# Optimization experiments

Hardware: AMD Instinct MI355X
Metric: run time of the kernel (lower is better)

The kernel has to match this reference:

```python
import jax, jax.numpy as jnp
import numpy as np

SIGMA = 0.05
KSIZE = 3
MIN_VAL = 50.0
MAX_VAL = 100.0


def _gauss_kernel():
    # ax = range(-(3//2)+1, 3//2+1) = [-1, 0, 1]  (matches TF int-floor-div)
    ax = jnp.arange(-(KSIZE // 2) + 1.0, KSIZE // 2 + 1.0)
    xx, yy = jnp.meshgrid(ax, ax)
    k = jnp.exp(-(xx ** 2 + yy ** 2) / (2.0 * SIGMA ** 2))
    k = k / jnp.sum(k)
    return k[..., None, None].astype(jnp.float32)  # HWIO, C=1


def _reflect_pad(x):
    return jnp.pad(x, ((0, 0), (1, 1), (1, 1), (0, 0)), mode='reflect')


def _conv(x, k):
    return jax.lax.conv_general_dilated(x, k, (1, 1), 'VALID',
                                        dimension_numbers=('NHWC', 'HWIO', 'NHWC'))


def _canny(images):
    blur = _conv(_reflect_pad(images), _gauss_kernel())
    h = jnp.array([[-1, 0, 1], [-2, 0, 2], [-1, 0, 1]], jnp.float32)[..., None, None]
    v = jnp.array([[-1, -2, -1], [0, 0, 0], [1, 2, 1]], jnp.float32)[..., None, None]
    bp = _reflect_pad(blur)
    gx = _conv(bp, h)
    gy = _conv(bp, v)
    gxy = jnp.sqrt(gx ** 2 + gy ** 2)
    # NOTE: original uses atan2(gx, gy) in this arg order
    theta = (jnp.arctan2(gx, gy) * (180.0 / np.pi) + 90.0) % 180.0

    H, W = gx.shape[1], gx.shape[2]
    # dilation2d with a -inf/0 kernel == max over the kernel's zero-offsets of the
    # zero-padded image; offsets are (dy,dx) of the 0 entries of each 3x3 filter.
    offsets = [
        [(1, 0), (1, 1), (1, 2)],  # horizontal bin: middle row
        [(0, 2), (1, 1), (2, 0)],  # 45 deg: anti-diagonal
        [(0, 1), (1, 1), (2, 1)],  # vertical bin: middle column
        [(0, 0), (1, 1), (2, 2)],  # 135 deg: main diagonal
    ]
    conds = [
        jnp.logical_or(theta >= 157.5, theta < 22.5),
        jnp.logical_and(theta >= 22.5, theta < 67.5),
        jnp.logical_and(theta >= 67.5, theta < 112.5),
        jnp.logical_and(theta >= 112.5, theta < 157.5),
    ]

    edge = jnp.zeros_like(gxy)
    for cond, offs in zip(conds, offsets):
        ang = jnp.where(cond, gxy, 0.0)
        pad = jnp.pad(ang, ((0, 0), (1, 1), (1, 1), (0, 0)))  # zero pad, as ZeroPadding2D
        mp = pad[:, offs[0][0]:offs[0][0] + H, offs[0][1]:offs[0][1] + W, :]
        for dy, dx in offs[1:]:
            mp = jnp.maximum(mp, pad[:, dy:dy + H, dx:dx + W, :])
        edge = edge + jnp.where(mp == ang, ang, 0.0)

    edge_sure = jnp.where(edge >= MAX_VAL, 255.0, 0.0)
    edge_week = jnp.where(jnp.logical_and(edge >= MIN_VAL, edge < MAX_VAL), 255.0, 0.0)
    edge_image = jnp.where(jnp.logical_or(edge_week == 255.0, edge_sure == 255.0), 255.5, 0.0)
    return edge_image, edge_week, edge_sure


def setup_inputs() -> dict:
    key = jax.random.key(0)
    images = jax.random.uniform(key, (16, 1024, 1024, 1), dtype=jnp.float32) * 255.0
    return {"images": images}


def reference(images):
    return _canny(images)
```

## Files before the change

### kernel.cpp

```cpp
#include <hip/hip_runtime.h>
#include <math.h>

#define IMG_H 1024
#define IMG_W 1024
#define OUT_H 1025
#define OUT_W 1025
#define NIMG  16
#define TOTAL (NIMG * OUT_H * OUT_W)

#define TILE_W 64
#define TILE_H 16
#define HALO_W 68
#define HALO_H 18
#define NQX    17
#define NQUAD  (HALO_H * NQX)
#define NTHREADS 320

__device__ __forceinline__ int refl(int k) {
    if (k >= 2) return (k <= 1025) ? (k - 2) : 1022;
    return k;
}

__device__ __forceinline__ void sobel_generic(const float* __restrict__ img, int i, int j,
                                              float& gx, float& gy) {
    int r0 = refl(i), r1 = refl(i + 1), r2 = refl(i + 2);
    int c0 = refl(j), c1 = refl(j + 1), c2 = refl(j + 2);
    const float* p0 = img + r0 * IMG_W;
    const float* p1 = img + r1 * IMG_W;
    const float* p2 = img + r2 * IMG_W;
    float v00 = p0[c0], v01 = p0[c1], v02 = p0[c2];
    float v10 = p1[c0],               v12 = p1[c2];
    float v20 = p2[c0], v21 = p2[c1], v22 = p2[c2];

    float t = -v00;
    t = __fadd_rn(t, v02);
    t = __fadd_rn(t, -2.0f * v10);
    t = __fadd_rn(t, 2.0f * v12);
    t = __fadd_rn(t, -v20);
    gx = __fadd_rn(t, v22);

    t = -v00;
    t = __fadd_rn(t, -2.0f * v01);
    t = __fadd_rn(t, -v02);
    t = __fadd_rn(t, v20);
    t = __fadd_rn(t, 2.0f * v21);
    gy = __fadd_rn(t, v22);
}

__device__ int classify_slow(float gx, float gy) {
    float t = (float)atan2((double)gx, (double)gy);
    float deg = __fmul_rn(t, (float)(180.0 / M_PI));
    float th = __fadd_rn(deg, 90.0f);
    th = fmodf(th, 180.0f);
    if (th < 0.0f) th += 180.0f;
    if (th < 22.5f || th >= 157.5f) return 0;
    if (th < 67.5f) return 1;
    if (th < 112.5f) return 2;
    return 3;
}

__device__ __forceinline__ int classify(float gx, float gy) {
    float ax = fabsf(gx), ay = fabsf(gy);
    const float T22_LO = 0.414172141e0f;
    const float T22_HI = 0.414254984e0f;
    const float T67_LO = 2.413972141e0f;
    const float T67_HI = 2.414454984e0f;

    if (ax <= ay * T22_LO) return 2;
    if (ax >= ay * T67_HI) return 0;
    if (ax >= ay * T22_HI && ax <= ay * T67_LO) {
        unsigned s = (__float_as_uint(gx) ^ __float_as_uint(gy)) >> 31;
        return s ? 1 : 3;
    }
    return classify_slow(gx, gy);
}

__device__ __forceinline__ float mag(float gx, float gy) {
    return __fsqrt_rn(__fadd_rn(__fmul_rn(gx, gx), __fmul_rn(gy, gy)));
}

__device__ __forceinline__ void load6(const float* __restrict__ p, float v[6]) {
    float4 a = *(const float4*)p;
    float2 b = *(const float2*)(p + 4);
    v[0] = a.x; v[1] = a.y; v[2] = a.z; v[3] = a.w; v[4] = b.x; v[5] = b.y;
}

__global__ __launch_bounds__(NTHREADS) void canny_kernel(const float* __restrict__ images,
                                                         float* __restrict__ out) {
    __shared__ float    g_s[HALO_H * HALO_W];
    __shared__ unsigned b_u[HALO_H * NQX];

    const int tile_ox = blockIdx.x * TILE_W;
    const int tile_oy = blockIdx.y * TILE_H;
    const int n       = blockIdx.z;
    const float* img = images + (size_t)n * IMG_H * IMG_W;
    const int t = threadIdx.x;

    if (t < NQUAD) {
        int hy  = t / NQX;
        int qx  = t - hy * NQX;
        int oy  = tile_oy + hy - 1;
        int ox0 = tile_ox + qx * 4 - 2;

        float    gq[4];
        unsigned bq[4];

        if (oy >= 2 && oy <= 1023 && ox0 >= 2 && ox0 <= 1020) {
            const float* r0p = img + (oy - 2) * IMG_W + (ox0 - 2);
            float R0[6], R1[6], R2[6];
            load6(r0p, R0);
            load6(r0p + IMG_W, R1);
            load6(r0p + 2 * IMG_W, R2);
            #pragma unroll
            for (int p = 0; p < 4; p++) {
                float v00 = R0[p], v01 = R0[p + 1], v02 = R0[p + 2];
                float v10 = R1[p],                  v12 = R1[p + 2];
                float v20 = R2[p], v21 = R2[p + 1], v22 = R2[p + 2];

                float s = -v00;
                s = __fadd_rn(s, v02);
                s = __fadd_rn(s, -2.0f * v10);
                s = __fadd_rn(s, 2.0f * v12);
                s = __fadd_rn(s, -v20);
                float gx = __fadd_rn(s, v22);

                s = -v00;
                s = __fadd_rn(s, -2.0f * v01);
                s = __fadd_rn(s, -v02);
                s = __fadd_rn(s, v20);
                s = __fadd_rn(s, 2.0f * v21);
                float gy = __fadd_rn(s, v22);

                gq[p] = mag(gx, gy);
                bq[p] = (unsigned)classify(gx, gy);
            }
        } else {
            #pragma unroll
            for (int p = 0; p < 4; p++) {
                int ox = ox0 + p;
                float g = -1.0f;
                unsigned b = 255u;
                if (oy >= 0 && oy < OUT_H && ox >= 0 && ox < OUT_W) {
                    float gx, gy;
                    sobel_generic(img, oy, ox, gx, gy);
                    g = mag(gx, gy);
                    b = (unsigned)classify(gx, gy);
                }
                gq[p] = g;
                bq[p] = b;
            }
        }

        int ldoff = hy * HALO_W + qx * 4;
        *(float4*)&g_s[ldoff] = make_float4(gq[0], gq[1], gq[2], gq[3]);
        b_u[hy * NQX + qx] = bq[0] | (bq[1] << 8) | (bq[2] << 16) | (bq[3] << 24);
    }
    __syncthreads();

    const unsigned char* b_s = (const unsigned char*)b_u;
    #pragma unroll
    for (int q = 0; q < 4; q++) {
        int p = t + NTHREADS * q;
        if (p >= TILE_W * TILE_H) break;
        int r = p >> 6, c = p & 63;
        int oy = tile_oy + r, ox = tile_ox + c;
        if (oy >= OUT_H || ox >= OUT_W) continue;

        int hc = (r + 1) * HALO_W + (c + 2);
        float gc = g_s[hc];
        int   bc = b_s[hc];

        int doff = (bc == 0) ? 1
                 : (bc == 1) ? (HALO_W - 1)
                 : (bc == 2) ? HALO_W
                 :             (HALO_W + 1);

        float nmax = 0.0f;
        float g1 = g_s[hc + doff];
        if (b_s[hc + doff] == bc && g1 > nmax) nmax = g1;
        float g2 = g_s[hc - doff];
        if (b_s[hc - doff] == bc && g2 > nmax) nmax = g2;

        float e = (gc >= nmax) ? gc : 0.0f;

        size_t o = (size_t)(n * OUT_H + oy) * OUT_W + ox;
        out[o]                       = (e >= 50.0f) ? 255.5f : 0.0f;
        out[(size_t)TOTAL + o]       = (e >= 50.0f && e < 100.0f) ? 255.0f : 0.0f;
        out[(size_t)(2 * TOTAL) + o] = (e >= 100.0f) ? 255.0f : 0.0f;
    }
}

extern "C" void kernel_launch(void* const* d_in, const int* in_sizes, int n_in,
                              void* d_out, int out_size, void* d_ws, size_t ws_size,
                              hipStream_t stream) {
    const float* images = (const float*)d_in[0];
    float* out = (float*)d_out;
    dim3 grid((OUT_W + TILE_W - 1) / TILE_W,
              (OUT_H + TILE_H - 1) / TILE_H,
              NIMG);
    canny_kernel<<<grid, NTHREADS, 0, stream>>>(images, out);
}
```

Before: 297.8 us.

## Compute two Sobel rows per thread and vectorize NMS phase over 4 pixels

Each producer thread now loads four input rows and computes gradient magnitude and bin for two halo rows, reusing the shared middle rows. This cuts global loads per gradient and lowers the thread count to 256. The NMS phase has each thread handle four consecutive pixels: it reads float4 magnitudes and packed bin words from shared memory and picks neighbors with selects instead of per-pixel scattered byte loads. The classify function is restructured so the slow atan2 path is a single unlikely branch. The trade-off is more registers per thread and only 153 of 256 threads active in the gradient phase.

```diff
diff --git a/kernel.cpp b/kernel.cpp
--- a/kernel.cpp
+++ b/kernel.cpp
@@ -6,15 +6,15 @@
 #define OUT_H 1025
 #define OUT_W 1025
 #define NIMG  16
-#define TOTAL (NIMG * OUT_H * OUT_W)
+#define TOTAL ((size_t)NIMG * OUT_H * OUT_W)
 
 #define TILE_W 64
 #define TILE_H 16
 #define HALO_W 68
 #define HALO_H 18
 #define NQX    17
-#define NQUAD  (HALO_H * NQX)
-#define NTHREADS 320
+#define NPAIRS 9
+#define NMT    (NQX * NPAIRS)
 
 __device__ __forceinline__ int refl(int k) {
     if (k >= 2) return (k <= 1025) ? (k - 2) : 1022;
@@ -47,6 +47,28 @@
     gy = __fadd_rn(t, v22);
 }
 
+__device__ __forceinline__ void sobel_rows(const float R0[6], const float R1[6],
+                                           const float R2[6], int p,
+                                           float& gx, float& gy) {
+    float v00 = R0[p], v01 = R0[p + 1], v02 = R0[p + 2];
+    float v10 = R1[p],                  v12 = R1[p + 2];
+    float v20 = R2[p], v21 = R2[p + 1], v22 = R2[p + 2];
+
+    float s = -v00;
+    s = __fadd_rn(s, v02);
+    s = __fadd_rn(s, -2.0f * v10);
+    s = __fadd_rn(s, 2.0f * v12);
+    s = __fadd_rn(s, -v20);
+    gx = __fadd_rn(s, v22);
+
+    s = -v00;
+    s = __fadd_rn(s, -2.0f * v01);
+    s = __fadd_rn(s, -v02);
+    s = __fadd_rn(s, v20);
+    s = __fadd_rn(s, 2.0f * v21);
+    gy = __fadd_rn(s, v22);
+}
+
 __device__ int classify_slow(float gx, float gy) {
     float t = (float)atan2((double)gx, (double)gy);
     float deg = __fmul_rn(t, (float)(180.0 / M_PI));
@@ -66,13 +88,14 @@
     const float T67_LO = 2.413972141e0f;
     const float T67_HI = 2.414454984e0f;
 
-    if (ax <= ay * T22_LO) return 2;
-    if (ax >= ay * T67_HI) return 0;
-    if (ax >= ay * T22_HI && ax <= ay * T67_LO) {
-        unsigned s = (__float_as_uint(gx) ^ __float_as_uint(gy)) >> 31;
-        return s ? 1 : 3;
-    }
-    return classify_slow(gx, gy);
+    bool in22 = (ax > ay * T22_LO) && (ax < ay * T22_HI);
+    bool in67 = (ax > ay * T67_LO) && (ax < ay * T67_HI);
+    if (__builtin_expect(in22 || in67, 0))
+        return classify_slow(gx, gy);
+
+    unsigned s = (__float_as_uint(gx) ^ __float_as_uint(gy)) >> 31;
+    int diag = s ? 1 : 3;
+    return (ax <= ay * T22_LO) ? 2 : ((ax >= ay * T67_HI) ? 0 : diag);
 }
 
 __device__ __forceinline__ float mag(float gx, float gy) {
@@ -85,8 +108,12 @@
     v[0] = a.x; v[1] = a.y; v[2] = a.z; v[3] = a.w; v[4] = b.x; v[5] = b.y;
 }
 
-__global__ __launch_bounds__(NTHREADS) void canny_kernel(const float* __restrict__ images,
-                                                         float* __restrict__ out) {
+__device__ __forceinline__ unsigned byteN(unsigned wa, unsigned wb, int k) {
+    return (k < 4) ? ((wa >> (8 * k)) & 0xffu) : ((wb >> (8 * (k - 4))) & 0xffu);
+}
+
+__global__ __launch_bounds__(256) void canny_kernel(const float* __restrict__ images,
+                                                    float* __restrict__ out) {
     __shared__ float    g_s[HALO_H * HALO_W];
     __shared__ unsigned b_u[HALO_H * NQX];
 
@@ -96,97 +123,129 @@
     const float* img = images + (size_t)n * IMG_H * IMG_W;
     const int t = threadIdx.x;
 
-    if (t < NQUAD) {
-        int hy  = t / NQX;
-        int qx  = t - hy * NQX;
-        int oy  = tile_oy + hy - 1;
+    if (t < NMT) {
+        int my  = t / NQX;
+        int qx  = t - my * NQX;
+        int hy0 = my * 2;
+        int oy0 = tile_oy + hy0 - 1;
         int ox0 = tile_ox + qx * 4 - 2;
 
-        float    gq[4];
-        unsigned bq[4];
-
-        if (oy >= 2 && oy <= 1023 && ox0 >= 2 && ox0 <= 1020) {
-            const float* r0p = img + (oy - 2) * IMG_W + (ox0 - 2);
-            float R0[6], R1[6], R2[6];
-            load6(r0p, R0);
-            load6(r0p + IMG_W, R1);
-            load6(r0p + 2 * IMG_W, R2);
+        float    gq[2][4];
+        unsigned bq[2][4];
+
+        if (oy0 >= 2 && oy0 <= 1022 && ox0 >= 2 && ox0 <= 1020) {
+            const float* rp = img + (oy0 - 2) * IMG_W + (ox0 - 2);
+            float R[4][6];
+            load6(rp,               R[0]);
+            load6(rp + IMG_W,       R[1]);
+            load6(rp + 2 * IMG_W,   R[2]);
+            load6(rp + 3 * IMG_W,   R[3]);
             #pragma unroll
-            for (int p = 0; p < 4; p++) {
-                float v00 = R0[p], v01 = R0[p + 1], v02 = R0[p + 2];
-                float v10 = R1[p],                  v12 = R1[p + 2];
-                float v20 = R2[p], v21 = R2[p + 1], v22 = R2[p + 2];
-
-                float s = -v00;
-                s = __fadd_rn(s, v02);
-                s = __fadd_rn(s, -2.0f * v10);
-                s = __fadd_rn(s, 2.0f * v12);
-                s = __fadd_rn(s, -v20);
-                float gx = __fadd_rn(s, v22);
-
-                s = -v00;
-                s = __fadd_rn(s, -2.0f * v01);
-                s = __fadd_rn(s, -v02);
-                s = __fadd_rn(s, v20);
-                s = __fadd_rn(s, 2.0f * v21);
-                float gy = __fadd_rn(s, v22);
-
-                gq[p] = mag(gx, gy);
-                bq[p] = (unsigned)classify(gx, gy);
+            for (int rr = 0; rr < 2; rr++) {
+                #pragma unroll
+                for (int p = 0; p < 4; p++) {
+                    float gx, gy;
+                    sobel_rows(R[rr], R[rr + 1], R[rr + 2], p, gx, gy);
+                    gq[rr][p] = mag(gx, gy);
+                    bq[rr][p] = (unsigned)classify(gx, gy);
+                }
             }
         } else {
             #pragma unroll
-            for (int p = 0; p < 4; p++) {
-                int ox = ox0 + p;
-                float g = -1.0f;
-                unsigned b = 255u;
-                if (oy >= 0 && oy < OUT_H && ox >= 0 && ox < OUT_W) {
-                    float gx, gy;
-                    sobel_generic(img, oy, ox, gx, gy);
-                    g = mag(gx, gy);
-                    b = (unsigned)classify(gx, gy);
+            for (int rr = 0; rr < 2; rr++) {
+                #pragma unroll
+                for (int p = 0; p < 4; p++) {
+                    int oy = oy0 + rr, ox = ox0 + p;
+                    float g = -1.0f;
+                    unsigned b = 255u;
+                    if (oy >= 0 && oy < OUT_H && ox >= 0 && ox < OUT_W) {
+                        float gx, gy;
+                        sobel_generic(img, oy, ox, gx, gy);
+                        g = mag(gx, gy);
+                        b = (unsigned)classify(gx, gy);
+                    }
+                    gq[rr][p] = g;
+                    bq[rr][p] = b;
                 }
-                gq[p] = g;
-                bq[p] = b;
             }
         }
 
-        int ldoff = hy * HALO_W + qx * 4;
-        *(float4*)&g_s[ldoff] = make_float4(gq[0], gq[1], gq[2], gq[3]);
-        b_u[hy * NQX + qx] = bq[0] | (bq[1] << 8) | (bq[2] << 16) | (bq[3] << 24);
+        #pragma unroll
+        for (int rr = 0; rr < 2; rr++) {
+            *(float4*)&g_s[(hy0 + rr) * HALO_W + qx * 4] =
+                make_float4(gq[rr][0], gq[rr][1], gq[rr][2], gq[rr][3]);
+            b_u[(hy0 + rr) * NQX + qx] =
+                bq[rr][0] | (bq[rr][1] << 8) | (bq[rr][2] << 16) | (bq[rr][3] << 24);
+        }
     }
     __syncthreads();
 
-    const unsigned char* b_s = (const unsigned char*)b_u;
-    #pragma unroll
-    for (int q = 0; q < 4; q++) {
-        int p = t + NTHREADS * q;
-        if (p >= TILE_W * TILE_H) break;
-        int r = p >> 6, c = p & 63;
-        int oy = tile_oy + r, ox = tile_ox + c;
-        if (oy >= OUT_H || ox >= OUT_W) continue;
-
-        int hc = (r + 1) * HALO_W + (c + 2);
-        float gc = g_s[hc];
-        int   bc = b_s[hc];
-
-        int doff = (bc == 0) ? 1
-                 : (bc == 1) ? (HALO_W - 1)
-                 : (bc == 2) ? HALO_W
-                 :             (HALO_W + 1);
-
-        float nmax = 0.0f;
-        float g1 = g_s[hc + doff];
-        if (b_s[hc + doff] == bc && g1 > nmax) nmax = g1;
-        float g2 = g_s[hc - doff];
-        if (b_s[hc - doff] == bc && g2 > nmax) nmax = g2;
-
-        float e = (gc >= nmax) ? gc : 0.0f;
-
-        size_t o = (size_t)(n * OUT_H + oy) * OUT_W + ox;
-        out[o]                       = (e >= 50.0f) ? 255.5f : 0.0f;
-        out[(size_t)TOTAL + o]       = (e >= 50.0f && e < 100.0f) ? 255.0f : 0.0f;
-        out[(size_t)(2 * TOTAL) + o] = (e >= 100.0f) ? 255.0f : 0.0f;
+    {
+        int r  = t >> 4;
+        int qx = t & 15;
+        int c  = qx * 4;
+        int oy = tile_oy + r;
+
+        int base = r * HALO_W + c;
+        float4 a0 = *(const float4*)&g_s[base];
+        float4 a1 = *(const float4*)&g_s[base + 4];
+        float4 b0 = *(const float4*)&g_s[base + HALO_W];
+        float4 b1 = *(const float4*)&g_s[base + HALO_W + 4];
+        float4 c0 = *(const float4*)&g_s[base + 2 * HALO_W];
+        float4 c1 = *(const float4*)&g_s[base + 2 * HALO_W + 4];
+        float G0[8] = {a0.x, a0.y, a0.z, a0.w, a1.x, a1.y, a1.z, a1.w};
+        float G1[8] = {b0.x, b0.y, b0.z, b0.w, b1.x, b1.y, b1.z, b1.w};
+        float G2[8] = {c0.x, c0.y, c0.z, c0.w, c1.x, c1.y, c1.z, c1.w};
+
+        unsigned B0a = b_u[r * NQX + qx],       B0b = b_u[r * NQX + qx + 1];
+        unsigned B1a = b_u[(r + 1) * NQX + qx], B1b = b_u[(r + 1) * NQX + qx + 1];
+        unsigned B2a = b_u[(r + 2) * NQX + qx], B2b = b_u[(r + 2) * NQX + qx + 1];
+
+        float vi[4], vw[4], vs[4];
+        #pragma unroll
+        for (int p = 0; p < 4; p++) {
+            float    gc = G1[2 + p];
+            unsigned bc = byteN(B1a, B1b, 2 + p);
+
+            float n1 = (bc == 0) ? G1[3 + p]
+                     : (bc == 1) ? G2[1 + p]
+                     : (bc == 2) ? G2[2 + p]
+                     :             G2[3 + p];
+            unsigned b1 = (bc == 0) ? byteN(B1a, B1b, 3 + p)
+                        : (bc == 1) ? byteN(B2a, B2b, 1 + p)
+                        : (bc == 2) ? byteN(B2a, B2b, 2 + p)
+                        :             byteN(B2a, B2b, 3 + p);
+            float n2 = (bc == 0) ? G1[1 + p]
+                     : (bc == 1) ? G0[3 + p]
+                     : (bc == 2) ? G0[2 + p]
+                     :             G0[1 + p];
+            unsigned b2 = (bc == 0) ? byteN(B1a, B1b, 1 + p)
+                        : (bc == 1) ? byteN(B0a, B0b, 3 + p)
+                        : (bc == 2) ? byteN(B0a, B0b, 2 + p)
+                        :             byteN(B0a, B0b, 1 + p);
+
+            float m1 = (b1 == bc) ? n1 : 0.0f;
+            float m2 = (b2 == bc) ? n2 : 0.0f;
+            float nmax = fmaxf(m1, m2);
+            float e = (gc >= nmax) ? gc : 0.0f;
+
+            vi[p] = (e >= 50.0f) ? 255.5f : 0.0f;
+            vw[p] = (e >= 50.0f && e < 100.0f) ? 255.0f : 0.0f;
+            vs[p] = (e >= 100.0f) ? 255.0f : 0.0f;
+        }
+
+        if (oy < OUT_H) {
+            size_t o = (size_t)(n * OUT_H + oy) * OUT_W + (tile_ox + c);
+            #pragma unroll
+            for (int p = 0; p < 4; p++) {
+                int ox = tile_ox + c + p;
+                if (ox < OUT_W) {
+                    out[o + p]             = vi[p];
+                    out[TOTAL + o + p]     = vw[p];
+                    out[2 * TOTAL + o + p] = vs[p];
+                }
+            }
+        }
     }
 }
 
@@ -198,5 +257,5 @@
     dim3 grid((OUT_W + TILE_W - 1) / TILE_W,
               (OUT_H + TILE_H - 1) / TILE_H,
               NIMG);
-    canny_kernel<<<grid, NTHREADS, 0, stream>>>(images, out);
-}
+    canny_kernel<<<grid, 256, 0, stream>>>(images, out);
+}
```

Result: slower. 334.9 us (+12.5%).
